# Optimization experiments

Hardware: AMD Instinct MI355X
Metric: run time of the kernel (lower is better)

The kernel has to match this reference:

```python
import jax, jax.numpy as jnp
import numpy as np

OUT_FEATURES = 4096
IN_FEATURES = 4096
GROUP_SIZE = 128


def setup_inputs() -> dict:
    key = jax.random.key(0)
    k1, k2, k3, k4, k5 = jax.random.split(key, 5)
    x = jax.random.normal(k1, (4, 2048, IN_FEATURES), dtype=jnp.float32)
    # two 4-bit codes per byte-like int32 element
    packed = jax.random.randint(k2, (OUT_FEATURES * IN_FEATURES // 2,), 0, 256, dtype=jnp.int32)
    n_groups = OUT_FEATURES * IN_FEATURES // GROUP_SIZE
    scales = jax.random.uniform(k3, (n_groups,), dtype=jnp.float32) * 0.02 + 1e-3
    offsets = jax.random.normal(k4, (n_groups,), dtype=jnp.float32) * 0.01
    bias = jax.random.normal(k5, (OUT_FEATURES,), dtype=jnp.float32)
    return {"x": x, "packed": packed, "scales": scales, "offsets": offsets, "bias": bias}


def _dequant(packed, scales, offsets):
    # unpack low/high nibbles -> int codes in [0, 15]
    low = packed & 0xF
    high = (packed >> 4) & 0xF
    codes = jnp.stack([low, high], axis=-1).reshape(-1).astype(jnp.float32)  # [out*in]
    # per-group affine dequant: w = code * scale + offset
    w = codes.reshape(-1, GROUP_SIZE) * scales[:, None] + offsets[:, None]
    return w.reshape(OUT_FEATURES, IN_FEATURES)


def reference(x, packed, scales, offsets, bias):
    weight = _dequant(packed, scales, offsets)  # [out, in]
    # F.linear: x @ W^T + b
    return jnp.einsum('bsi,oi->bso', x, weight) + bias
```

## Files before the change

kernel.cpp:

```cpp
#include <hip/hip_runtime.h>
#include <stdint.h>

#define IN_F   4096
#define OUT_F  4096
#define M_TOT  8192
#define BK     64
#define NT2    (IN_F / BK)
#define HBUF   65536

typedef __bf16 bf16x8 __attribute__((ext_vector_type(8)));
typedef float  floatx4 __attribute__((ext_vector_type(4)));

#define WAITVM(N) asm volatile("s_waitcnt vmcnt(" #N ")" ::: "memory")
#define LG() do {                                      \
    asm volatile("s_waitcnt lgkmcnt(0)" ::: "memory"); \
    __builtin_amdgcn_sched_barrier(0);                 \
} while (0)
#define FB() do {                                     \
    asm volatile("" ::: "memory");                    \
    __builtin_amdgcn_s_barrier();                     \
    asm volatile("" ::: "memory");                    \
    __builtin_amdgcn_sched_barrier(0);                \
} while (0)

__device__ __forceinline__ unsigned short f2bf_bits(float f) {
    union { float f; uint32_t u; } v; v.f = f;
    uint32_t r = v.u + 0x7FFF + ((v.u >> 16) & 1);
    return (unsigned short)(r >> 16);
}

__device__ __forceinline__ void gl_lds16(const void* g, void* l) {
    __builtin_amdgcn_global_load_lds(
        (const __attribute__((address_space(1))) void*)g,
        (__attribute__((address_space(3))) void*)l, 16, 0, 0);
}

__global__ void cvt_x_kernel(const float* __restrict__ x, ushort* __restrict__ xb) {
    int i = blockIdx.x * blockDim.x + threadIdx.x;
    const float4* xp = reinterpret_cast<const float4*>(x);
    float4 a = xp[2 * i], b = xp[2 * i + 1];
    uint4 o;
    o.x = (uint32_t)f2bf_bits(a.x) | ((uint32_t)f2bf_bits(a.y) << 16);
    o.y = (uint32_t)f2bf_bits(a.z) | ((uint32_t)f2bf_bits(a.w) << 16);
    o.z = (uint32_t)f2bf_bits(b.x) | ((uint32_t)f2bf_bits(b.y) << 16);
    o.w = (uint32_t)f2bf_bits(b.z) | ((uint32_t)f2bf_bits(b.w) << 16);
    reinterpret_cast<uint4*>(xb)[i] = o;
}

__global__ void dequant_kernel(const int* __restrict__ packed,
                               const float* __restrict__ scales,
                               const float* __restrict__ offsets,
                               ushort* __restrict__ wb) {
    int i = blockIdx.x * blockDim.x + threadIdx.x;
    int4 p = reinterpret_cast<const int4*>(packed)[i];
    int g = i >> 4;
    float s = scales[g], off = offsets[g];
    uint4 ov;
    {
        int pv = p.x;
        unsigned w0 = f2bf_bits((float)(pv & 0xF) * s + off);
        unsigned w1 = f2bf_bits((float)((pv >> 4) & 0xF) * s + off);
        ov.x = w0 | (w1 << 16);
    }
    {
        int pv = p.y;
        unsigned w0 = f2bf_bits((float)(pv & 0xF) * s + off);
        unsigned w1 = f2bf_bits((float)((pv >> 4) & 0xF) * s + off);
        ov.y = w0 | (w1 << 16);
    }
    {
        int pv = p.z;
        unsigned w0 = f2bf_bits((float)(pv & 0xF) * s + off);
        unsigned w1 = f2bf_bits((float)((pv >> 4) & 0xF) * s + off);
        ov.z = w0 | (w1 << 16);
    }
    {
        int pv = p.w;
        unsigned w0 = f2bf_bits((float)(pv & 0xF) * s + off);
        unsigned w1 = f2bf_bits((float)((pv >> 4) & 0xF) * s + off);
        ov.w = w0 | (w1 << 16);
    }
    reinterpret_cast<uint4*>(wb)[i] = ov;
}

__launch_bounds__(512, 2)
__global__ void gemm_kernel(const ushort* __restrict__ A,
                            const ushort* __restrict__ B,
                            const float* __restrict__ bias,
                            float* __restrict__ C) {
    __shared__ __align__(16) char smem[2 * HBUF];

    const int tid  = threadIdx.x;
    const int wave = tid >> 6;
    const int lane = tid & 63;
    const int quad = lane >> 4;
    const int l16  = lane & 15;
    const int wm   = wave >> 2;
    const int wn   = wave & 3;

    int id = blockIdx.y * gridDim.x + blockIdx.x;
    id = (id & 7) * 64 + (id >> 3);
    const int bn = id & 15;
    const int bm = id >> 4;

    const int rbase = tid >> 2;
    const int scol  = ((tid & 3) << 4) ^ (((rbase >> 1) & 3) << 4);
    const ushort* pA = A + (size_t)(bm * 256 + rbase) * IN_F + (scol >> 1);
    const ushort* pB = B + (size_t)(bn * 256 + rbase) * IN_F + (scol >> 1);
    const int ldsw = wave * 1024;

    auto STG = [&](const ushort* g, char* subblk, int eo) {
        gl_lds16(g + eo, subblk + ldsw);
        gl_lds16(g + eo + (size_t)128 * IN_F, subblk + 8192 + ldsw);
    };

    const int arow0 = wm * 128 + l16;
    const int brow0 = wn * 64 + l16;
    const int acol = (((quad << 4) ^ (((arow0 >> 1) & 3) << 4)) >> 1);
    const int bcol = (((quad << 4) ^ (((brow0 >> 1) & 3) << 4)) >> 1);

    floatx4 acc[8][4] = {};
    bf16x8 a8[8], bb[4];

    auto RDA = [&](const ushort* bufp, int ks) {
#pragma unroll
        for (int mi = 0; mi < 8; ++mi)
            a8[mi] = *reinterpret_cast<const bf16x8*>(
                bufp + ks * 8192 + (arow0 + mi * 16) * 32 + acol);
    };
    auto RDB = [&](const ushort* bufp, int ks, int nh) {
#pragma unroll
        for (int ni = 0; ni < 2; ++ni)
            bb[nh * 2 + ni] = *reinterpret_cast<const bf16x8*>(
                bufp + 16384 + ks * 8192 + (brow0 + (nh * 2 + ni) * 16) * 32 + bcol);
    };

#define MFMA16(NH) do {                                                   \
    __builtin_amdgcn_s_setprio(1);                                        \
    _Pragma("unroll")                                                     \
    for (int mi = 0; mi < 8; ++mi)                                        \
        _Pragma("unroll")                                                 \
        for (int ni = 0; ni < 2; ++ni)                                    \
            acc[mi][(NH) * 2 + ni] =                                      \
                __builtin_amdgcn_mfma_f32_16x16x32_bf16(                  \
                    a8[mi], bb[(NH) * 2 + ni], acc[mi][(NH) * 2 + ni],    \
                    0, 0, 0);                                             \
    __builtin_amdgcn_s_setprio(0);                                        \
} while (0)

#define TILE_MAIN(CB, SB, ts) do {                                        \
    const ushort* bp_ = (const ushort*)(smem + (CB));                     \
    char* aS_ = smem + (SB);                                              \
    char* bS_ = smem + (SB) + 32768;                                      \
    const int eo_ = (ts) * 64;                                            \
    RDA(bp_, 0); RDB(bp_, 0, 0); STG(pB, bS_, eo_);                       \
    FB(); LG(); MFMA16(0); FB();                                          \
    RDB(bp_, 0, 1); STG(pA, aS_, eo_); WAITVM(4);                         \
    FB(); LG(); MFMA16(1); FB();                                          \
    RDA(bp_, 1); RDB(bp_, 1, 0); STG(pB, bS_ + 16384, eo_ + 32);          \
    FB(); LG(); MFMA16(0); FB();                                          \
    RDB(bp_, 1, 1); STG(pA, aS_ + 16384, eo_ + 32); WAITVM(4);            \
    FB(); LG(); MFMA16(1); FB();                                          \
} while (0)

#define TILE_LAST(CB) do {                                                \
    const ushort* bp_ = (const ushort*)(smem + (CB));                     \
    RDA(bp_, 0); RDB(bp_, 0, 0); FB(); LG(); MFMA16(0); FB();             \
    RDB(bp_, 0, 1); WAITVM(0);   FB(); LG(); MFMA16(1); FB();             \
    RDA(bp_, 1); RDB(bp_, 1, 0); FB(); LG(); MFMA16(0); FB();             \
    RDB(bp_, 1, 1); LG(); MFMA16(1);                                      \
} while (0)

    STG(pB, smem + 32768, 0);
    STG(pA, smem, 0);
    STG(pB, smem + 32768 + 16384, 32);
    STG(pA, smem + 16384, 32);
    WAITVM(4);
    FB();

#pragma unroll 1
    for (int t = 0; t < NT2 - 2; t += 2) {
        TILE_MAIN(0,    HBUF, t + 1);
        TILE_MAIN(HBUF, 0,    t + 2);
    }
    TILE_MAIN(0, HBUF, NT2 - 1);
    TILE_LAST(HBUF);

#undef TILE_MAIN
#undef TILE_LAST
#undef MFMA16

    const int ccol = bn * 256 + wn * 64 + l16;
    const float* bp = bias + ccol;
    float* Cp = C + (size_t)(bm * 256 + wm * 128 + quad * 4) * OUT_F + ccol;
#pragma unroll
    for (int mi = 0; mi < 8; ++mi) {
#pragma unroll
        for (int ni = 0; ni < 4; ++ni) {
            float bv = bp[ni * 16];
#pragma unroll
            for (int r = 0; r < 4; ++r)
                Cp[(size_t)(mi * 16 + r) * OUT_F + ni * 16] = acc[mi][ni][r] + bv;
        }
    }
}

extern "C" void kernel_launch(void* const* d_in, const int* in_sizes, int n_in,
                              void* d_out, int out_size, void* d_ws, size_t ws_size,
                              hipStream_t stream) {
    const float* x       = (const float*)d_in[0];
    const int*   packed  = (const int*)d_in[1];
    const float* scales  = (const float*)d_in[2];
    const float* offsets = (const float*)d_in[3];
    const float* bias    = (const float*)d_in[4];
    float* out = (float*)d_out;

    ushort* xb = (ushort*)d_ws;
    ushort* wb = (ushort*)((char*)d_ws + (size_t)M_TOT * IN_F * 2);

    cvt_x_kernel<<<16384, 256, 0, stream>>>(x, xb);
    dequant_kernel<<<8192, 256, 0, stream>>>(packed, scales, offsets, wb);

    dim3 grid(OUT_F / 256, M_TOT / 256);
    gemm_kernel<<<grid, 512, 0, stream>>>(xb, wb, bias, out);
}
```

Before: 484.4 us.

## Fuse x conversion and weight dequantization into GEMM tile loads

Removes the separate fp32->bf16 conversion and 4-bit dequant kernels and performs both inside the GEMM. Each tile is loaded through registers, converted, and written to LDS, with prefetch one tile ahead. This avoids writing and re-reading the bf16 intermediates in global memory. In exchange, every block redoes conversion and dequant work, it reads fp32 x at twice the byte width, and it loses the direct global-to-LDS loads and the finer-grained pipeline schedule.

```diff
diff --git a/kernel.cpp b/kernel.cpp
--- a/kernel.cpp
+++ b/kernel.cpp
@@ -6,12 +6,12 @@
 #define M_TOT  8192
 #define BK     64
 #define NT2    (IN_F / BK)
+#define ABUF   32768
 #define HBUF   65536
 
 typedef __bf16 bf16x8 __attribute__((ext_vector_type(8)));
 typedef float  floatx4 __attribute__((ext_vector_type(4)));
 
-#define WAITVM(N) asm volatile("s_waitcnt vmcnt(" #N ")" ::: "memory")
 #define LG() do {                                      \
     asm volatile("s_waitcnt lgkmcnt(0)" ::: "memory"); \
     __builtin_amdgcn_sched_barrier(0);                 \
@@ -29,65 +29,19 @@
     return (unsigned short)(r >> 16);
 }
 
-__device__ __forceinline__ void gl_lds16(const void* g, void* l) {
-    __builtin_amdgcn_global_load_lds(
-        (const __attribute__((address_space(1))) void*)g,
-        (__attribute__((address_space(3))) void*)l, 16, 0, 0);
-}
-
-__global__ void cvt_x_kernel(const float* __restrict__ x, ushort* __restrict__ xb) {
-    int i = blockIdx.x * blockDim.x + threadIdx.x;
-    const float4* xp = reinterpret_cast<const float4*>(x);
-    float4 a = xp[2 * i], b = xp[2 * i + 1];
-    uint4 o;
-    o.x = (uint32_t)f2bf_bits(a.x) | ((uint32_t)f2bf_bits(a.y) << 16);
-    o.y = (uint32_t)f2bf_bits(a.z) | ((uint32_t)f2bf_bits(a.w) << 16);
-    o.z = (uint32_t)f2bf_bits(b.x) | ((uint32_t)f2bf_bits(b.y) << 16);
-    o.w = (uint32_t)f2bf_bits(b.z) | ((uint32_t)f2bf_bits(b.w) << 16);
-    reinterpret_cast<uint4*>(xb)[i] = o;
-}
-
-__global__ void dequant_kernel(const int* __restrict__ packed,
-                               const float* __restrict__ scales,
-                               const float* __restrict__ offsets,
-                               ushort* __restrict__ wb) {
-    int i = blockIdx.x * blockDim.x + threadIdx.x;
-    int4 p = reinterpret_cast<const int4*>(packed)[i];
-    int g = i >> 4;
-    float s = scales[g], off = offsets[g];
-    uint4 ov;
-    {
-        int pv = p.x;
-        unsigned w0 = f2bf_bits((float)(pv & 0xF) * s + off);
-        unsigned w1 = f2bf_bits((float)((pv >> 4) & 0xF) * s + off);
-        ov.x = w0 | (w1 << 16);
-    }
-    {
-        int pv = p.y;
-        unsigned w0 = f2bf_bits((float)(pv & 0xF) * s + off);
-        unsigned w1 = f2bf_bits((float)((pv >> 4) & 0xF) * s + off);
-        ov.y = w0 | (w1 << 16);
-    }
-    {
-        int pv = p.z;
-        unsigned w0 = f2bf_bits((float)(pv & 0xF) * s + off);
-        unsigned w1 = f2bf_bits((float)((pv >> 4) & 0xF) * s + off);
-        ov.z = w0 | (w1 << 16);
-    }
-    {
-        int pv = p.w;
-        unsigned w0 = f2bf_bits((float)(pv & 0xF) * s + off);
-        unsigned w1 = f2bf_bits((float)((pv >> 4) & 0xF) * s + off);
-        ov.w = w0 | (w1 << 16);
-    }
-    reinterpret_cast<uint4*>(wb)[i] = ov;
+__device__ __forceinline__ unsigned int pack2(int v, float s, float o) {
+    unsigned int w0 = f2bf_bits((float)(v & 0xF) * s + o);
+    unsigned int w1 = f2bf_bits((float)((v >> 4) & 0xF) * s + o);
+    return w0 | (w1 << 16);
 }
 
 __launch_bounds__(512, 2)
-__global__ void gemm_kernel(const ushort* __restrict__ A,
-                            const ushort* __restrict__ B,
-                            const float* __restrict__ bias,
-                            float* __restrict__ C) {
+__global__ void gemm_fused_kernel(const float* __restrict__ X,
+                                  const int*   __restrict__ P,
+                                  const float* __restrict__ S,
+                                  const float* __restrict__ Ofs,
+                                  const float* __restrict__ bias,
+                                  float* __restrict__ C) {
     __shared__ __align__(16) char smem[2 * HBUF];
 
     const int tid  = threadIdx.x;
@@ -103,15 +57,57 @@
     const int bn = id & 15;
     const int bm = id >> 4;
 
-    const int rbase = tid >> 2;
-    const int scol  = ((tid & 3) << 4) ^ (((rbase >> 1) & 3) << 4);
-    const ushort* pA = A + (size_t)(bm * 256 + rbase) * IN_F + (scol >> 1);
-    const ushort* pB = B + (size_t)(bn * 256 + rbase) * IN_F + (scol >> 1);
-    const int ldsw = wave * 1024;
+    const int a_r0 = tid >> 4;
+    const int a_c4 = (tid & 15) << 2;
+    const float* gx = X + (size_t)(bm * 256 + a_r0) * IN_F + a_c4;
+    const int a_ks = a_c4 >> 5;
+    const int a_bc = ((a_c4 & 31) << 1) ^ (((a_r0 >> 1) & 3) << 4);
 
-    auto STG = [&](const ushort* g, char* subblk, int eo) {
-        gl_lds16(g + eo, subblk + ldsw);
-        gl_lds16(g + eo + (size_t)128 * IN_F, subblk + 8192 + ldsw);
+    const int b_r0 = tid >> 3;
+    const int b_i4 = (tid & 7) << 2;
+    const int* gp = P + (size_t)(bn * 256 + b_r0) * (IN_F / 2) + b_i4;
+    const int b_ks = (tid & 7) >> 2;
+    const int b_bc = (((tid & 7) & 3) << 4) ^ (((b_r0 >> 1) & 3) << 4);
+    const int b_g0 = (bn * 256 + b_r0) * 32;
+
+    float4 sA[8]; int4 sB[4]; float sS[4], sO[4];
+
+    auto ISSUE = [&](int t) {
+        const int K0 = t * BK;
+#pragma unroll
+        for (int j = 0; j < 8; ++j)
+            sA[j] = *reinterpret_cast<const float4*>(gx + K0 + (size_t)j * 32 * IN_F);
+#pragma unroll
+        for (int j = 0; j < 4; ++j)
+            sB[j] = *reinterpret_cast<const int4*>(gp + K0 / 2 + (size_t)j * 64 * (IN_F / 2));
+#pragma unroll
+        for (int j = 0; j < 4; ++j) {
+            sS[j] = S[b_g0 + j * 2048 + (t >> 1)];
+            sO[j] = Ofs[b_g0 + j * 2048 + (t >> 1)];
+        }
+    };
+
+    auto CVTWRITE = [&](char* buf) {
+        char* Ab = buf + a_ks * 16384;
+#pragma unroll
+        for (int j = 0; j < 8; ++j) {
+            const int rj = a_r0 + j * 32;
+            uint2 w;
+            w.x = (unsigned)f2bf_bits(sA[j].x) | ((unsigned)f2bf_bits(sA[j].y) << 16);
+            w.y = (unsigned)f2bf_bits(sA[j].z) | ((unsigned)f2bf_bits(sA[j].w) << 16);
+            *reinterpret_cast<uint2*>(Ab + rj * 64 + a_bc) = w;
+        }
+        char* Bb = buf + ABUF + b_ks * 16384;
+#pragma unroll
+        for (int j = 0; j < 4; ++j) {
+            const int rj = b_r0 + j * 64;
+            uint4 w;
+            w.x = pack2(sB[j].x, sS[j], sO[j]);
+            w.y = pack2(sB[j].y, sS[j], sO[j]);
+            w.z = pack2(sB[j].z, sS[j], sO[j]);
+            w.w = pack2(sB[j].w, sS[j], sO[j]);
+            *reinterpret_cast<uint4*>(Bb + rj * 64 + b_bc) = w;
+        }
     };
 
     const int arow0 = wm * 128 + l16;
@@ -120,74 +116,49 @@
     const int bcol = (((quad << 4) ^ (((brow0 >> 1) & 3) << 4)) >> 1);
 
     floatx4 acc[8][4] = {};
-    bf16x8 a8[8], bb[4];
+    bf16x8 a4[4], bb[4];
 
-    auto RDA = [&](const ushort* bufp, int ks) {
+    auto RDA = [&](const ushort* bufp, int ks, int mh) {
 #pragma unroll
-        for (int mi = 0; mi < 8; ++mi)
-            a8[mi] = *reinterpret_cast<const bf16x8*>(
-                bufp + ks * 8192 + (arow0 + mi * 16) * 32 + acol);
+        for (int mi = 0; mi < 4; ++mi)
+            a4[mi] = *reinterpret_cast<const bf16x8*>(
+                bufp + ks * 8192 + (arow0 + (mh * 4 + mi) * 16) * 32 + acol);
     };
-    auto RDB = [&](const ushort* bufp, int ks, int nh) {
+    auto RDB = [&](const ushort* bufp, int ks) {
 #pragma unroll
-        for (int ni = 0; ni < 2; ++ni)
-            bb[nh * 2 + ni] = *reinterpret_cast<const bf16x8*>(
-                bufp + 16384 + ks * 8192 + (brow0 + (nh * 2 + ni) * 16) * 32 + bcol);
+        for (int ni = 0; ni < 4; ++ni)
+            bb[ni] = *reinterpret_cast<const bf16x8*>(
+                bufp + 16384 + ks * 8192 + (brow0 + ni * 16) * 32 + bcol);
     };
 
-#define MFMA16(NH) do {                                                   \
-    __builtin_amdgcn_s_setprio(1);                                        \
-    _Pragma("unroll")                                                     \
-    for (int mi = 0; mi < 8; ++mi)                                        \
-        _Pragma("unroll")                                                 \
-        for (int ni = 0; ni < 2; ++ni)                                    \
-            acc[mi][(NH) * 2 + ni] =                                      \
-                __builtin_amdgcn_mfma_f32_16x16x32_bf16(                  \
-                    a8[mi], bb[(NH) * 2 + ni], acc[mi][(NH) * 2 + ni],    \
-                    0, 0, 0);                                             \
-    __builtin_amdgcn_s_setprio(0);                                        \
+#define MFMA16(MH) do {                                              \
+    __builtin_amdgcn_s_setprio(1);                                   \
+    _Pragma("unroll")                                                \
+    for (int mi = 0; mi < 4; ++mi)                                   \
+        _Pragma("unroll")                                            \
+        for (int ni = 0; ni < 4; ++ni)                               \
+            acc[(MH) * 4 + mi][ni] =                                 \
+                __builtin_amdgcn_mfma_f32_16x16x32_bf16(             \
+                    a4[mi], bb[ni], acc[(MH) * 4 + mi][ni], 0, 0, 0);\
+    __builtin_amdgcn_s_setprio(0);                                   \
 } while (0)
 
-#define TILE_MAIN(CB, SB, ts) do {                                        \
-    const ushort* bp_ = (const ushort*)(smem + (CB));                     \
-    char* aS_ = smem + (SB);                                              \
-    char* bS_ = smem + (SB) + 32768;                                      \
-    const int eo_ = (ts) * 64;                                            \
-    RDA(bp_, 0); RDB(bp_, 0, 0); STG(pB, bS_, eo_);                       \
-    FB(); LG(); MFMA16(0); FB();                                          \
-    RDB(bp_, 0, 1); STG(pA, aS_, eo_); WAITVM(4);                         \
-    FB(); LG(); MFMA16(1); FB();                                          \
-    RDA(bp_, 1); RDB(bp_, 1, 0); STG(pB, bS_ + 16384, eo_ + 32);          \
-    FB(); LG(); MFMA16(0); FB();                                          \
-    RDB(bp_, 1, 1); STG(pA, aS_ + 16384, eo_ + 32); WAITVM(4);            \
-    FB(); LG(); MFMA16(1); FB();                                          \
-} while (0)
-
-#define TILE_LAST(CB) do {                                                \
-    const ushort* bp_ = (const ushort*)(smem + (CB));                     \
-    RDA(bp_, 0); RDB(bp_, 0, 0); FB(); LG(); MFMA16(0); FB();             \
-    RDB(bp_, 0, 1); WAITVM(0);   FB(); LG(); MFMA16(1); FB();             \
-    RDA(bp_, 1); RDB(bp_, 1, 0); FB(); LG(); MFMA16(0); FB();             \
-    RDB(bp_, 1, 1); LG(); MFMA16(1);                                      \
-} while (0)
-
-    STG(pB, smem + 32768, 0);
-    STG(pA, smem, 0);
-    STG(pB, smem + 32768 + 16384, 32);
-    STG(pA, smem + 16384, 32);
-    WAITVM(4);
-    FB();
+    ISSUE(0);
+    CVTWRITE(smem);
+    ISSUE(1);
+    LG(); FB();
 
 #pragma unroll 1
-    for (int t = 0; t < NT2 - 2; t += 2) {
-        TILE_MAIN(0,    HBUF, t + 1);
-        TILE_MAIN(HBUF, 0,    t + 2);
+    for (int t = 0; t < NT2; ++t) {
+        if (t + 1 < NT2) CVTWRITE(smem + ((t + 1) & 1) * HBUF);
+        const ushort* bufp = (const ushort*)(smem + (t & 1) * HBUF);
+        RDB(bufp, 0); RDA(bufp, 0, 0); MFMA16(0);
+        RDA(bufp, 0, 1); MFMA16(1);
+        if (t + 2 < NT2) ISSUE(t + 2);
+        RDB(bufp, 1); RDA(bufp, 1, 0); MFMA16(0);
+        RDA(bufp, 1, 1); MFMA16(1);
+        LG(); FB();
     }
-    TILE_MAIN(0, HBUF, NT2 - 1);
-    TILE_LAST(HBUF);
-
-#undef TILE_MAIN
-#undef TILE_LAST
 #undef MFMA16
 
     const int ccol = bn * 256 + wn * 64 + l16;
@@ -215,12 +186,6 @@
     const float* bias    = (const float*)d_in[4];
     float* out = (float*)d_out;
 
-    ushort* xb = (ushort*)d_ws;
-    ushort* wb = (ushort*)((char*)d_ws + (size_t)M_TOT * IN_F * 2);
-
-    cvt_x_kernel<<<16384, 256, 0, stream>>>(x, xb);
-    dequant_kernel<<<8192, 256, 0, stream>>>(packed, scales, offsets, wb);
-
     dim3 grid(OUT_F / 256, M_TOT / 256);
-    gemm_kernel<<<grid, 512, 0, stream>>>(xb, wb, bias, out);
+    gemm_fused_kernel<<<grid, 512, 0, stream>>>(x, packed, scales, offsets, bias, out);
 }
```

New measurement: 632.9 us. +30.7%, slower.
